# Optimization experiments

Measured on AMD Instinct MI355X. Metric: run time of the kernel, lower is better.

Reference implementation:

```python
import jax, jax.numpy as jnp
import numpy as np

P = 2048       # output dim (genes)
D = 64         # latent dim
H1, H2 = 512, 512  # n_neurons
E = 16         # num_experts
N = 2048       # batch
GATE_H = 64    # gate hidden width


def _glorot(key, shape):
    fan_in, fan_out = shape[-2], shape[-1]
    lim = jnp.sqrt(6.0 / (fan_in + fan_out)).astype(jnp.float32)
    return jax.random.uniform(key, shape, jnp.float32, -lim, lim)


def setup_inputs() -> dict:
    key = jax.random.key(0)
    ks = jax.random.split(key, 12)
    z = jax.random.normal(ks[0], (N, D), jnp.float32)
    # stacked per-expert MLP weights: d -> H1 -> H2 -> p
    W1 = _glorot(ks[1], (E, D, H1));  b1 = jnp.zeros((E, H1), jnp.float32)
    W2 = _glorot(ks[2], (E, H1, H2)); b2 = jnp.zeros((E, H2), jnp.float32)
    W3 = _glorot(ks[3], (E, H2, P));  b3 = jnp.zeros((E, P), jnp.float32)
    # gate network: d -> 64 -> E
    Wg1 = _glorot(ks[4], (D, GATE_H)); bg1 = jnp.zeros((GATE_H,), jnp.float32)
    Wg2 = _glorot(ks[5], (GATE_H, E)); bg2 = jnp.zeros((E,), jnp.float32)
    # expert assignment matrix A: [p, E], binary; ensure no all-zero row
    u = jax.random.uniform(ks[6], (P, E))
    A = jnp.where(u < 0.5, 1.0, 0.0).astype(jnp.float32)
    A = A.at[:, 0].set(1.0)
    return {"z": z, "W1": W1, "b1": b1, "W2": W2, "b2": b2,
            "W3": W3, "b3": b3, "Wg1": Wg1, "bg1": bg1,
            "Wg2": Wg2, "bg2": bg2, "A": A}


def reference(z, W1, b1, W2, b2, W3, b3, Wg1, bg1, Wg2, bg2, A):
    # experts, batched across E (replaces Python loop over nn.ModuleList)
    h = jax.nn.relu(jnp.einsum('nd,edh->neh', z, W1) + b1[None])      # [N,E,H1]
    h = jax.nn.relu(jnp.einsum('neh,ehk->nek', h, W2) + b2[None])     # [N,E,H2]
    expert_out = jnp.einsum('nek,ekp->nep', h, W3) + b3[None]         # [N,E,P]
    # gate network + softmax over experts
    g = jax.nn.relu(z @ Wg1 + bg1) @ Wg2 + bg2                        # [N,E]
    gate = jax.nn.softmax(g, axis=1)                                  # [N,E]
    # feature-wise gating: gate[n,e] * A[p,e], normalized over experts
    fw = gate[:, None, :] * A[None, :, :]                             # [N,P,E]
    fw = fw / (jnp.sum(fw, axis=2, keepdims=True) + 1e-8)
    # weighted combine: sum_e expert_out[n,e,p] * fw[n,p,e]
    x_rec = jnp.einsum('nep,npe->np', expert_out, fw)                 # [N,P]
    return (x_rec, fw)
```

## Files before the change

kernel.cpp:

```cpp
#include <hip/hip_runtime.h>
#include <hip/hip_bf16.h>

#define NN   2048
#define DD   64
#define HH1  512
#define HH2  512
#define PP   2048
#define EE   16
#define KBIG (EE * HH2)

typedef unsigned short ushort_t;
typedef __attribute__((ext_vector_type(8))) short bf16x8;
typedef __attribute__((ext_vector_type(4))) float f32x4;

__device__ __forceinline__ float b2f(ushort_t u) {
  union { unsigned int i; float f; } v; v.i = ((unsigned int)u) << 16; return v.f;
}
__device__ __forceinline__ ushort_t f2b(float f) {
  union { float f; unsigned int i; } v; v.f = f;
  unsigned int x = v.i;
  unsigned int r = (x + 0x7fffu + ((x >> 16) & 1u)) >> 16;
  return (ushort_t)r;
}
__device__ __forceinline__ float ldf(const void* p, size_t i, int isb) {
  return isb ? b2f(((const ushort_t*)p)[i]) : ((const float*)p)[i];
}

__device__ __forceinline__ void async16(ushort_t* lds, const ushort_t* g) {
  __builtin_amdgcn_global_load_lds(
      (const __attribute__((address_space(1))) void*)g,
      (__attribute__((address_space(3))) void*)lds, 16, 0, 0);
}

__device__ __forceinline__ int xcd_swz(int orig, int nwg) {
  int q = nwg >> 3, r = nwg & 7;
  int xcd = orig & 7, loc = orig >> 3;
  return (xcd < r ? xcd * (q + 1) : r * (q + 1) + (xcd - r) * q) + loc;
}

__global__ void k_sniff(const unsigned int* __restrict__ zraw,
                        int* __restrict__ flag) {
  __shared__ int cnt[256];
  int t = threadIdx.x;
  int c = 0;
  for (int i = t; i < 1024; i += 256) {
    unsigned int u = zraw[i];
    unsigned int e = (u >> 7) & 0xFFu;
    c += (e >= 110u && e <= 135u) ? 1 : 0;
  }
  cnt[t] = c;
  __syncthreads();
  for (int s = 128; s > 0; s >>= 1) {
    if (t < s) cnt[t] += cnt[t + s];
    __syncthreads();
  }
  if (t == 0) *flag = (cnt[0] >= 512) ? 1 : 0;
}

__global__ void k_probe(int* __restrict__ mapflag) {
  __shared__ ushort_t Ap[16 * 32];
  __shared__ ushort_t Bp[16 * 32];
  int t = threadIdx.x;
  for (int i = t; i < 512; i += 64) {
    int r = i >> 5, k = i & 31;
    Ap[i] = f2b((float)((r + k) % 7));
    Bp[i] = f2b((float)((2 * r + k) % 5));
  }
  __syncthreads();
  int lr = t & 15, quad = t >> 4;
  bf16x8 a = *(const bf16x8*)&Ap[lr * 32 + quad * 8];
  bf16x8 b = *(const bf16x8*)&Bp[lr * 32 + quad * 8];
  f32x4 acc = {};
  acc = __builtin_amdgcn_mfma_f32_16x16x32_bf16(a, b, acc, 0, 0, 0);
  bool m0 = true, m1 = true;
  for (int r = 0; r < 4; ++r) {
    float r0 = 0.f, r1 = 0.f;
    for (int k = 0; k < 32; ++k) {
      r0 += (float)(((quad * 4 + r) + k) % 7) * (float)((2 * lr + k) % 5);
      r1 += (float)((lr + k) % 7) * (float)((2 * (quad * 4 + r) + k) % 5);
    }
    m0 &= fabsf(acc[r] - r0) < 0.5f;
    m1 &= fabsf(acc[r] - r1) < 0.5f;
  }
  unsigned long long b0 = __ballot(m0);
  unsigned long long b1 = __ballot(m1);
  if (t == 0) *mapflag = (b0 == ~0ULL) ? 0 : ((b1 == ~0ULL) ? 1 : 0);
}

__global__ void k_convert(const void* __restrict__ src,
                          ushort_t* __restrict__ dst, int n,
                          const int* __restrict__ flag) {
  int isb = *flag;
  int stride = gridDim.x * blockDim.x;
  for (int g = blockIdx.x * blockDim.x + threadIdx.x; g * 8 < n; g += stride) {
    int base = g * 8;
    ushort_t ov[8];
    if (isb) {
      *(uint4*)ov = *(const uint4*)((const ushort_t*)src + base);
    } else {
      const float* s = (const float*)src + base;
      float4 f0 = *(const float4*)s;
      float4 f1 = *(const float4*)(s + 4);
      ov[0] = f2b(f0.x); ov[1] = f2b(f0.y); ov[2] = f2b(f0.z); ov[3] = f2b(f0.w);
      ov[4] = f2b(f1.x); ov[5] = f2b(f1.y); ov[6] = f2b(f1.z); ov[7] = f2b(f1.w);
    }
    *(uint4*)(dst + base) = *(uint4*)ov;
  }
}

__global__ void k_transpose_cvt(const void* __restrict__ src_,
                                ushort_t* __restrict__ dst, int K, int H,
                                int ld_dst, long e_dst_off,
                                const void* __restrict__ Amask,
                                const int* __restrict__ flag) {
  __shared__ ushort_t tile[64][68];
  int isb = *flag;
  int e = blockIdx.z;
  size_t ebase = (size_t)e * K * H;
  dst += (size_t)e * e_dst_off;
  int h0 = blockIdx.x * 64, k0 = blockIdx.y * 64;
  int t = threadIdx.x;
#pragma unroll
  for (int it = 0; it < 2; ++it) {
    int c = it * 256 + t;
    int row = c >> 3, col = (c & 7) * 8;
    size_t idx = ebase + (size_t)(k0 + row) * H + h0 + col;
    ushort_t tmp[8];
    if (isb) {
      *(uint4*)tmp = *(const uint4*)((const ushort_t*)src_ + idx);
    } else {
      const float* s = (const float*)src_ + idx;
      float4 f0 = *(const float4*)s;
      float4 f1 = *(const float4*)(s + 4);
      tmp[0] = f2b(f0.x); tmp[1] = f2b(f0.y); tmp[2] = f2b(f0.z); tmp[3] = f2b(f0.w);
      tmp[4] = f2b(f1.x); tmp[5] = f2b(f1.y); tmp[6] = f2b(f1.z); tmp[7] = f2b(f1.w);
    }
#pragma unroll
    for (int j = 0; j < 8; ++j) tile[row][col + j] = tmp[j];
  }
  __syncthreads();
#pragma unroll
  for (int it = 0; it < 2; ++it) {
    int c = it * 256 + t;
    int row = c >> 3, col = (c & 7) * 8;
    ushort_t tmp[8];
#pragma unroll
    for (int j = 0; j < 8; ++j) tmp[j] = tile[col + j][row];
    if (Amask) {
      float a = ldf(Amask, (size_t)(h0 + row) * EE + e, isb);
#pragma unroll
      for (int j = 0; j < 8; ++j) tmp[j] = f2b(a * b2f(tmp[j]));
    }
    *(uint4*)(dst + (size_t)(h0 + row) * ld_dst + k0 + col) = *(uint4*)tmp;
  }
}

__global__ void k_gate(const void* __restrict__ z,
                       const void* __restrict__ Wg1,
                       const void* __restrict__ bg1,
                       const void* __restrict__ Wg2,
                       const void* __restrict__ bg2,
                       const int* __restrict__ flag,
                       float* __restrict__ gate) {
  __shared__ float sW1[64][65];
  __shared__ float sW2[64][16];
  __shared__ float sb1[64];
  __shared__ float sb2[16];
  __shared__ float sz[4][64];
  __shared__ float shid[4][64];
  __shared__ float sg[4][16];
  int isb = *flag;
  int t = threadIdx.x;
  for (int i = t; i < 64 * 64; i += 256) sW1[i >> 6][i & 63] = ldf(Wg1, i, isb);
  for (int i = t; i < 64 * 16; i += 256) sW2[i >> 4][i & 15] = ldf(Wg2, i, isb);
  if (t < 64) sb1[t] = ldf(bg1, t, isb);
  if (t < 16) sb2[t] = ldf(bg2, t, isb);
  int w = t >> 6, l = t & 63;
  int n = blockIdx.x * 4 + w;
  sz[w][l] = ldf(z, (size_t)n * DD + l, isb);
  __syncthreads();
  float acc = sb1[l];
#pragma unroll
  for (int d = 0; d < 64; ++d) acc += sz[w][d] * sW1[d][l];
  shid[w][l] = fmaxf(acc, 0.f);
  __syncthreads();
  if (l < 16) {
    float g = sb2[l];
#pragma unroll
    for (int j = 0; j < 64; ++j) g += shid[w][j] * sW2[j][l];
    sg[w][l] = g;
  }
  __syncthreads();
  if (l < 16) {
    float m = -1e30f;
    for (int e2 = 0; e2 < 16; ++e2) m = fmaxf(m, sg[w][e2]);
    float s = 0.f;
    for (int e2 = 0; e2 < 16; ++e2) s += __expf(sg[w][e2] - m);
    gate[(size_t)n * EE + l] = __expf(sg[w][l] - m) / s;
  }
}

__global__ __launch_bounds__(256) void k_gemm_bt_relu(
    const ushort_t* __restrict__ Aact, const ushort_t* __restrict__ Bt,
    const ushort_t* __restrict__ bias, ushort_t* __restrict__ Cout,
    int M, int K, int ldc,
    long a_stride_e, long b_stride_e, long bias_stride_e, long c_stride_e,
    const float* __restrict__ gs,
    const int* __restrict__ mapflag) {
  __shared__ ushort_t As[2][128 * 32];
  __shared__ ushort_t Bs[2][128 * 32];
  int e = blockIdx.z;
  Aact += (size_t)e * a_stride_e;
  Bt   += (size_t)e * b_stride_e;
  bias += (size_t)e * bias_stride_e;
  Cout += (size_t)e * c_stride_e;
  int nxy = gridDim.x * gridDim.y;
  int swz = xcd_swz(blockIdx.x + gridDim.x * blockIdx.y, nxy);
  int m0 = (swz / gridDim.x) * 128, n0 = (swz % gridDim.x) * 128;
  int t = threadIdx.x;
  int w = t >> 6, l = t & 63;
  int wm = (w >> 1) * 64, wn = (w & 1) * 64;
  int lr = l & 15, quad = l >> 4;
  int mf = *mapflag;

  f32x4 acc[4][4] = {};
#pragma unroll
  for (int it = 0; it < 2; ++it) {
    int c = it * 256 + t;
    int row = c >> 2, kk = (c & 3) * 8;
    async16(&As[0][row * 32 + kk], Aact + (size_t)(m0 + row) * K + kk);
    async16(&Bs[0][row * 32 + kk], Bt + (size_t)(n0 + row) * K + kk);
  }
  __syncthreads();
  int cur = 0;
  for (int k0 = 0; k0 < K; k0 += 32) {
    if (k0 + 32 < K) {
      int nxt = cur ^ 1;
#pragma unroll
      for (int it = 0; it < 2; ++it) {
        int c = it * 256 + t;
        int row = c >> 2, kk = (c & 3) * 8;
        async16(&As[nxt][row * 32 + kk],
                Aact + (size_t)(m0 + row) * K + k0 + 32 + kk);
        async16(&Bs[nxt][row * 32 + kk],
                Bt + (size_t)(n0 + row) * K + k0 + 32 + kk);
      }
    }
    bf16x8 af[4], bfr[4];
#pragma unroll
    for (int i = 0; i < 4; ++i)
      af[i] = *(const bf16x8*)&As[cur][(wm + i * 16 + lr) * 32 + quad * 8];
#pragma unroll
    for (int j = 0; j < 4; ++j)
      bfr[j] = *(const bf16x8*)&Bs[cur][(wn + j * 16 + lr) * 32 + quad * 8];
#pragma unroll
    for (int i = 0; i < 4; ++i)
#pragma unroll
      for (int j = 0; j < 4; ++j)
        acc[i][j] = __builtin_amdgcn_mfma_f32_16x16x32_bf16(af[i], bfr[j],
                                                            acc[i][j], 0, 0, 0);
    __syncthreads();
    cur ^= 1;
  }
  if (mf == 0) {
    float gv[4][4];
#pragma unroll
    for (int i = 0; i < 4; ++i)
#pragma unroll
      for (int r = 0; r < 4; ++r)
        gv[i][r] = gs ? gs[(size_t)(m0 + wm + i * 16 + quad * 4 + r) * EE + e]
                      : 1.f;
#pragma unroll
    for (int j = 0; j < 4; ++j) {
      int n = n0 + wn + j * 16 + lr;
      float bv = b2f(bias[n]);
#pragma unroll
      for (int i = 0; i < 4; ++i)
#pragma unroll
        for (int r = 0; r < 4; ++r) {
          int m = m0 + wm + i * 16 + quad * 4 + r;
          Cout[(size_t)m * ldc + n] =
              f2b(fmaxf(acc[i][j][r] + bv, 0.f) * gv[i][r]);
        }
    }
  } else {
#pragma unroll
    for (int i = 0; i < 4; ++i) {
      int m = m0 + wm + i * 16 + lr;
      float gvi = gs ? gs[(size_t)m * EE + e] : 1.f;
#pragma unroll
      for (int j = 0; j < 4; ++j)
#pragma unroll
        for (int r = 0; r < 4; ++r) {
          int n = n0 + wn + j * 16 + quad * 4 + r;
          Cout[(size_t)m * ldc + n] =
              f2b(fmaxf(acc[i][j][r] + b2f(bias[n]), 0.f) * gvi);
        }
    }
  }
}

__global__ __launch_bounds__(256) void k_bigk(
    const ushort_t* __restrict__ Ab,
    const ushort_t* __restrict__ Bb,
    float* __restrict__ part,
    int splits,
    const int* __restrict__ mapflag) {
  __shared__ ushort_t As[2][128 * 32];
  __shared__ ushort_t Bs[2][128 * 32];
  int s = blockIdx.z;
  int nxy = gridDim.x * gridDim.y;
  int swz = xcd_swz(blockIdx.x + gridDim.x * blockIdx.y, nxy);
  int m0 = (swz / gridDim.x) * 128, n0 = (swz % gridDim.x) * 128;
  int t = threadIdx.x;
  int w = t >> 6, l = t & 63;
  int wm = (w >> 1) * 64, wn = (w & 1) * 64;
  int lr = l & 15, quad = l >> 4;
  int mf = *mapflag;
  float* out = part + (size_t)s * NN * PP;
  int kspan = KBIG / splits;
  int kbeg = s * kspan, kend = kbeg + kspan;

  f32x4 acc[4][4] = {};
#pragma unroll
  for (int it = 0; it < 2; ++it) {
    int c = it * 256 + t;
    int row = c >> 2, kk = (c & 3) * 8;
    async16(&As[0][row * 32 + kk], Ab + (size_t)(m0 + row) * KBIG + kbeg + kk);
    async16(&Bs[0][row * 32 + kk], Bb + (size_t)(n0 + row) * KBIG + kbeg + kk);
  }
  __syncthreads();
  int cur = 0;
  for (int k0 = kbeg; k0 < kend; k0 += 32) {
    if (k0 + 32 < kend) {
      int nxt = cur ^ 1;
#pragma unroll
      for (int it = 0; it < 2; ++it) {
        int c = it * 256 + t;
        int row = c >> 2, kk = (c & 3) * 8;
        async16(&As[nxt][row * 32 + kk],
                Ab + (size_t)(m0 + row) * KBIG + k0 + 32 + kk);
        async16(&Bs[nxt][row * 32 + kk],
                Bb + (size_t)(n0 + row) * KBIG + k0 + 32 + kk);
      }
    }
    bf16x8 af[4], bfr[4];
#pragma unroll
    for (int i = 0; i < 4; ++i)
      af[i] = *(const bf16x8*)&As[cur][(wm + i * 16 + lr) * 32 + quad * 8];
#pragma unroll
    for (int j = 0; j < 4; ++j)
      bfr[j] = *(const bf16x8*)&Bs[cur][(wn + j * 16 + lr) * 32 + quad * 8];
#pragma unroll
    for (int i = 0; i < 4; ++i)
#pragma unroll
      for (int j = 0; j < 4; ++j)
        acc[i][j] = __builtin_amdgcn_mfma_f32_16x16x32_bf16(af[i], bfr[j],
                                                            acc[i][j], 0, 0, 0);
    __syncthreads();
    cur ^= 1;
  }
  if (mf == 0) {
#pragma unroll
    for (int j = 0; j < 4; ++j) {
      int n = n0 + wn + j * 16 + lr;
#pragma unroll
      for (int i = 0; i < 4; ++i)
#pragma unroll
        for (int r = 0; r < 4; ++r) {
          int m = m0 + wm + i * 16 + quad * 4 + r;
          out[(size_t)m * PP + n] = acc[i][j][r];
        }
    }
  } else {
#pragma unroll
    for (int i = 0; i < 4; ++i) {
      int m = m0 + wm + i * 16 + lr;
#pragma unroll
      for (int j = 0; j < 4; ++j)
#pragma unroll
        for (int r = 0; r < 4; ++r) {
          int n = n0 + wn + j * 16 + quad * 4 + r;
          out[(size_t)m * PP + n] = acc[i][j][r];
        }
    }
  }
}

__global__ __launch_bounds__(256) void k_fw_final(
    const float* __restrict__ gate,
    const ushort_t* __restrict__ Amat,
    const ushort_t* __restrict__ b3,
    const float* __restrict__ part,
    int splits,
    float* __restrict__ xrec,
    float* __restrict__ fw) {
  size_t stride = (size_t)gridDim.x * blockDim.x;
  for (size_t i = (size_t)blockIdx.x * blockDim.x + threadIdx.x;
       i < (size_t)NN * PP; i += stride) {
    int n = (int)(i >> 11);
    int p = (int)(i & (PP - 1));
    uint4 a0 = *(const uint4*)(Amat + (size_t)p * EE);
    uint4 a1 = *(const uint4*)(Amat + (size_t)p * EE + 8);
    ushort_t av[16];
    *(uint4*)av = a0;
    *(uint4*)(av + 8) = a1;
    float wv[16];
    float s = 0.f, bias = 0.f;
#pragma unroll
    for (int e = 0; e < 16; ++e) {
      wv[e] = gate[(size_t)n * EE + e] * b2f(av[e]);
      s += wv[e];
      bias += wv[e] * b2f(b3[(size_t)e * PP + p]);
    }
    float num = bias;
    for (int sp = 0; sp < splits; ++sp) num += part[(size_t)sp * NN * PP + i];
    float inv = 1.f / (s + 1e-8f);
    xrec[i] = num * inv;
    float* dst = fw + i * EE;
#pragma unroll
    for (int e = 0; e < 16; ++e) wv[e] *= inv;
    *(float4*)(dst + 0)  = *(float4*)(wv + 0);
    *(float4*)(dst + 4)  = *(float4*)(wv + 4);
    *(float4*)(dst + 8)  = *(float4*)(wv + 8);
    *(float4*)(dst + 12) = *(float4*)(wv + 12);
  }
}

extern "C" void kernel_launch(void* const* d_in, const int* in_sizes, int n_in,
                              void* d_out, int out_size, void* d_ws,
                              size_t ws_size, hipStream_t stream) {
  const void* z_r   = d_in[0];
  const void* W1_r  = d_in[1];
  const void* b1_r  = d_in[2];
  const void* W2_r  = d_in[3];
  const void* b2_r  = d_in[4];
  const void* W3_r  = d_in[5];
  const void* b3_r  = d_in[6];
  const void* Wg1_r = d_in[7];
  const void* bg1_r = d_in[8];
  const void* Wg2_r = d_in[9];
  const void* bg2_r = d_in[10];
  const void* A_r   = d_in[11];

  float* xrec = (float*)d_out;
  float* fw   = (float*)d_out + (size_t)NN * PP;

  char* ws = (char*)d_ws;
  int* flag    = (int*)ws;             ws += 128;
  int* mapflag = (int*)ws;             ws += 128;
  float* gate = (float*)ws;            ws += (size_t)NN * EE * 4;
  ushort_t* zC   = (ushort_t*)ws;      ws += (size_t)NN * DD * 2;
  ushort_t* b1C  = (ushort_t*)ws;      ws += (size_t)EE * HH1 * 2;
  ushort_t* b2C  = (ushort_t*)ws;      ws += (size_t)EE * HH2 * 2;
  ushort_t* b3C  = (ushort_t*)ws;      ws += (size_t)EE * PP * 2;
  ushort_t* AC   = (ushort_t*)ws;      ws += (size_t)PP * EE * 2;
  ushort_t* W1t = (ushort_t*)ws;       ws += (size_t)EE * HH1 * DD * 2;
  ushort_t* W2t = (ushort_t*)ws;       ws += (size_t)EE * HH2 * HH1 * 2;
  ushort_t* W3big = (ushort_t*)ws;     ws += (size_t)PP * KBIG * 2;
  ushort_t* H2big = (ushort_t*)ws;     ws += (size_t)NN * KBIG * 2;
  ushort_t* h1  = (ushort_t*)ws;       ws += (size_t)EE * NN * HH1 * 2;
  float* partial = (float*)h1;
  size_t off_h1 = (size_t)((char*)h1 - (char*)d_ws);
  int splits = (ws_size >= off_h1 + (size_t)4 * NN * PP * 4) ? 4 : 2;

  k_sniff<<<1, 256, 0, stream>>>((const unsigned int*)z_r, flag);
  k_probe<<<1, 64, 0, stream>>>(mapflag);

  auto cvt = [&](const void* src, ushort_t* dst, int n) {
    int blocks = (n / 8 + 255) / 256;
    if (blocks < 1) blocks = 1;
    k_convert<<<blocks, 256, 0, stream>>>(src, dst, n, flag);
  };
  cvt(z_r,  zC,  NN * DD);
  cvt(b1_r, b1C, EE * HH1);
  cvt(b2_r, b2C, EE * HH2);
  cvt(b3_r, b3C, EE * PP);
  cvt(A_r,  AC,  PP * EE);

  k_transpose_cvt<<<dim3(HH1 / 64, DD / 64, EE), 256, 0, stream>>>(
      W1_r, W1t, DD, HH1, DD, (long)HH1 * DD, nullptr, flag);
  k_transpose_cvt<<<dim3(HH2 / 64, HH1 / 64, EE), 256, 0, stream>>>(
      W2_r, W2t, HH1, HH2, HH1, (long)HH2 * HH1, nullptr, flag);
  k_transpose_cvt<<<dim3(PP / 64, HH2 / 64, EE), 256, 0, stream>>>(
      W3_r, W3big, HH2, PP, KBIG, (long)HH2, A_r, flag);

  k_gate<<<NN / 4, 256, 0, stream>>>(z_r, Wg1_r, bg1_r, Wg2_r, bg2_r, flag, gate);

  k_gemm_bt_relu<<<dim3(HH1 / 128, NN / 128, EE), 256, 0, stream>>>(
      zC, W1t, b1C, h1, NN, DD, HH1,
      0, (long)HH1 * DD, HH1, (long)NN * HH1, nullptr, mapflag);
  k_gemm_bt_relu<<<dim3(HH2 / 128, NN / 128, EE), 256, 0, stream>>>(
      h1, W2t, b2C, H2big, NN, HH1, KBIG,
      (long)NN * HH1, (long)HH2 * HH1, HH2, (long)HH2, gate, mapflag);

  k_bigk<<<dim3(PP / 128, NN / 128, splits), 256, 0, stream>>>(
      H2big, W3big, partial, splits, mapflag);

  k_fw_final<<<2048, 256, 0, stream>>>(
      gate, AC, b3C, partial, splits, xrec, fw);
}
```

Measured before the change: 610.2 us.

## Use 256x256 tiles for big GEMMs, merge setup kernels, drop double buffering

```diff
diff --git a/kernel.cpp b/kernel.cpp
--- a/kernel.cpp
+++ b/kernel.cpp
@@ -32,15 +32,11 @@
       (__attribute__((address_space(3))) void*)lds, 16, 0, 0);
 }
 
-__device__ __forceinline__ int xcd_swz(int orig, int nwg) {
-  int q = nwg >> 3, r = nwg & 7;
-  int xcd = orig & 7, loc = orig >> 3;
-  return (xcd < r ? xcd * (q + 1) : r * (q + 1) + (xcd - r) * q) + loc;
-}
-
-__global__ void k_sniff(const unsigned int* __restrict__ zraw,
-                        int* __restrict__ flag) {
+__global__ void k_init(const unsigned int* __restrict__ zraw,
+                       int* __restrict__ flag, int* __restrict__ mapflag) {
   __shared__ int cnt[256];
+  __shared__ ushort_t Ap[16 * 32];
+  __shared__ ushort_t Bp[16 * 32];
   int t = threadIdx.x;
   int c = 0;
   for (int i = t; i < 1024; i += 256) {
@@ -55,50 +51,65 @@
     __syncthreads();
   }
   if (t == 0) *flag = (cnt[0] >= 512) ? 1 : 0;
-}
-
-__global__ void k_probe(int* __restrict__ mapflag) {
-  __shared__ ushort_t Ap[16 * 32];
-  __shared__ ushort_t Bp[16 * 32];
-  int t = threadIdx.x;
-  for (int i = t; i < 512; i += 64) {
-    int r = i >> 5, k = i & 31;
-    Ap[i] = f2b((float)((r + k) % 7));
-    Bp[i] = f2b((float)((2 * r + k) % 5));
+  if (t < 64) {
+    for (int i = t; i < 512; i += 64) {
+      int r = i >> 5, k = i & 31;
+      Ap[i] = f2b((float)((r + k) % 7));
+      Bp[i] = f2b((float)((2 * r + k) % 5));
+    }
   }
   __syncthreads();
-  int lr = t & 15, quad = t >> 4;
-  bf16x8 a = *(const bf16x8*)&Ap[lr * 32 + quad * 8];
-  bf16x8 b = *(const bf16x8*)&Bp[lr * 32 + quad * 8];
-  f32x4 acc = {};
-  acc = __builtin_amdgcn_mfma_f32_16x16x32_bf16(a, b, acc, 0, 0, 0);
-  bool m0 = true, m1 = true;
-  for (int r = 0; r < 4; ++r) {
-    float r0 = 0.f, r1 = 0.f;
-    for (int k = 0; k < 32; ++k) {
-      r0 += (float)(((quad * 4 + r) + k) % 7) * (float)((2 * lr + k) % 5);
-      r1 += (float)((lr + k) % 7) * (float)((2 * (quad * 4 + r) + k) % 5);
-    }
-    m0 &= fabsf(acc[r] - r0) < 0.5f;
-    m1 &= fabsf(acc[r] - r1) < 0.5f;
-  }
-  unsigned long long b0 = __ballot(m0);
-  unsigned long long b1 = __ballot(m1);
-  if (t == 0) *mapflag = (b0 == ~0ULL) ? 0 : ((b1 == ~0ULL) ? 1 : 0);
-}
-
-__global__ void k_convert(const void* __restrict__ src,
-                          ushort_t* __restrict__ dst, int n,
-                          const int* __restrict__ flag) {
+  if (t < 64) {
+    int lr = t & 15, quad = t >> 4;
+    bf16x8 a = *(const bf16x8*)&Ap[lr * 32 + quad * 8];
+    bf16x8 b = *(const bf16x8*)&Bp[lr * 32 + quad * 8];
+    f32x4 acc = {};
+    acc = __builtin_amdgcn_mfma_f32_16x16x32_bf16(a, b, acc, 0, 0, 0);
+    bool m0 = true, m1 = true;
+    for (int r = 0; r < 4; ++r) {
+      float r0 = 0.f, r1 = 0.f;
+      for (int k = 0; k < 32; ++k) {
+        r0 += (float)(((quad * 4 + r) + k) % 7) * (float)((2 * lr + k) % 5);
+        r1 += (float)((lr + k) % 7) * (float)((2 * (quad * 4 + r) + k) % 5);
+      }
+      m0 &= fabsf(acc[r] - r0) < 0.5f;
+      m1 &= fabsf(acc[r] - r1) < 0.5f;
+    }
+    unsigned long long b0 = __ballot(m0);
+    unsigned long long b1 = __ballot(m1);
+    if (t == 0) *mapflag = (b0 == ~0ULL) ? 0 : ((b1 == ~0ULL) ? 1 : 0);
+  }
+}
+
+#define CVT_O1 (NN * DD)
+#define CVT_O2 (CVT_O1 + EE * HH1)
+#define CVT_O3 (CVT_O2 + EE * HH2)
+#define CVT_O4 (CVT_O3 + EE * PP)
+#define CVT_O5 (CVT_O4 + PP * EE)
+__global__ void k_convert5(const void* __restrict__ s0,
+                           const void* __restrict__ s1,
+                           const void* __restrict__ s2,
+                           const void* __restrict__ s3,
+                           const void* __restrict__ s4,
+                           ushort_t* __restrict__ dst,
+                           const int* __restrict__ flag) {
   int isb = *flag;
   int stride = gridDim.x * blockDim.x;
-  for (int g = blockIdx.x * blockDim.x + threadIdx.x; g * 8 < n; g += stride) {
+  for (int g = blockIdx.x * blockDim.x + threadIdx.x; g * 8 < CVT_O5;
+       g += stride) {
     int base = g * 8;
+    const void* src;
+    int off;
+    if (base < CVT_O1)      { src = s0; off = base; }
+    else if (base < CVT_O2) { src = s1; off = base - CVT_O1; }
+    else if (base < CVT_O3) { src = s2; off = base - CVT_O2; }
+    else if (base < CVT_O4) { src = s3; off = base - CVT_O3; }
+    else                    { src = s4; off = base - CVT_O4; }
     ushort_t ov[8];
     if (isb) {
-      *(uint4*)ov = *(const uint4*)((const ushort_t*)src + base);
+      *(uint4*)ov = *(const uint4*)((const ushort_t*)src + off);
     } else {
-      const float* s = (const float*)src + base;
+      const float* s = (const float*)src + off;
       float4 f0 = *(const float4*)s;
       float4 f1 = *(const float4*)(s + 4);
       ov[0] = f2b(f0.x); ov[1] = f2b(f0.y); ov[2] = f2b(f0.z); ov[3] = f2b(f0.w);
@@ -207,16 +218,14 @@
     long a_stride_e, long b_stride_e, long bias_stride_e, long c_stride_e,
     const float* __restrict__ gs,
     const int* __restrict__ mapflag) {
-  __shared__ ushort_t As[2][128 * 32];
-  __shared__ ushort_t Bs[2][128 * 32];
+  __shared__ ushort_t As[128 * 32];
+  __shared__ ushort_t Bs[128 * 32];
   int e = blockIdx.z;
   Aact += (size_t)e * a_stride_e;
   Bt   += (size_t)e * b_stride_e;
   bias += (size_t)e * bias_stride_e;
   Cout += (size_t)e * c_stride_e;
-  int nxy = gridDim.x * gridDim.y;
-  int swz = xcd_swz(blockIdx.x + gridDim.x * blockIdx.y, nxy);
-  int m0 = (swz / gridDim.x) * 128, n0 = (swz % gridDim.x) * 128;
+  int m0 = blockIdx.y * 128, n0 = blockIdx.x * 128;
   int t = threadIdx.x;
   int w = t >> 6, l = t & 63;
   int wm = (w >> 1) * 64, wn = (w & 1) * 64;
@@ -224,35 +233,27 @@
   int mf = *mapflag;
 
   f32x4 acc[4][4] = {};
-#pragma unroll
-  for (int it = 0; it < 2; ++it) {
-    int c = it * 256 + t;
-    int row = c >> 2, kk = (c & 3) * 8;
-    async16(&As[0][row * 32 + kk], Aact + (size_t)(m0 + row) * K + kk);
-    async16(&Bs[0][row * 32 + kk], Bt + (size_t)(n0 + row) * K + kk);
-  }
-  __syncthreads();
-  int cur = 0;
   for (int k0 = 0; k0 < K; k0 += 32) {
-    if (k0 + 32 < K) {
-      int nxt = cur ^ 1;
-#pragma unroll
-      for (int it = 0; it < 2; ++it) {
-        int c = it * 256 + t;
-        int row = c >> 2, kk = (c & 3) * 8;
-        async16(&As[nxt][row * 32 + kk],
-                Aact + (size_t)(m0 + row) * K + k0 + 32 + kk);
-        async16(&Bs[nxt][row * 32 + kk],
-                Bt + (size_t)(n0 + row) * K + k0 + 32 + kk);
-      }
-    }
+#pragma unroll
+    for (int it = 0; it < 2; ++it) {
+      int c = it * 256 + t;
+      int row = c >> 2, kk = (c & 3) * 8;
+      async16(&As[row * 32 + kk], Aact + (size_t)(m0 + row) * K + k0 + kk);
+    }
+#pragma unroll
+    for (int it = 0; it < 2; ++it) {
+      int c = it * 256 + t;
+      int row = c >> 2, kk = (c & 3) * 8;
+      async16(&Bs[row * 32 + kk], Bt + (size_t)(n0 + row) * K + k0 + kk);
+    }
+    __syncthreads();
     bf16x8 af[4], bfr[4];
 #pragma unroll
     for (int i = 0; i < 4; ++i)
-      af[i] = *(const bf16x8*)&As[cur][(wm + i * 16 + lr) * 32 + quad * 8];
+      af[i] = *(const bf16x8*)&As[(wm + i * 16 + lr) * 32 + quad * 8];
 #pragma unroll
     for (int j = 0; j < 4; ++j)
-      bfr[j] = *(const bf16x8*)&Bs[cur][(wn + j * 16 + lr) * 32 + quad * 8];
+      bfr[j] = *(const bf16x8*)&Bs[(wn + j * 16 + lr) * 32 + quad * 8];
 #pragma unroll
     for (int i = 0; i < 4; ++i)
 #pragma unroll
@@ -260,7 +261,6 @@
         acc[i][j] = __builtin_amdgcn_mfma_f32_16x16x32_bf16(af[i], bfr[j],
                                                             acc[i][j], 0, 0, 0);
     __syncthreads();
-    cur ^= 1;
   }
   if (mf == 0) {
     float gv[4][4];
@@ -300,81 +300,160 @@
   }
 }
 
-__global__ __launch_bounds__(256) void k_bigk(
+
+#define STAGE256(dstLDS, srcBase, ldK)                                       \
+  {                                                                          \
+    _Pragma("unroll") for (int it = 0; it < 4; ++it) {                       \
+      int c = it * 512 + t;                                                  \
+      int row = c >> 3, kk = (c & 7) * 8;                                    \
+      async16(&dstLDS[row * 64 + kk], srcBase + (size_t)row * ldK + kk);     \
+    }                                                                        \
+  }
+
+__global__ __launch_bounds__(512) void k_gemm256_relu(
+    const ushort_t* __restrict__ Aact, const ushort_t* __restrict__ Bt,
+    const ushort_t* __restrict__ bias, ushort_t* __restrict__ Cout,
+    int K, int ldc,
+    long a_stride_e, long b_stride_e, long bias_stride_e, long c_stride_e,
+    const float* __restrict__ gs,
+    const int* __restrict__ mapflag) {
+  __shared__ ushort_t As[256 * 64];
+  __shared__ ushort_t Bs[256 * 64];
+  int e = blockIdx.z;
+  Aact += (size_t)e * a_stride_e;
+  Bt   += (size_t)e * b_stride_e;
+  bias += (size_t)e * bias_stride_e;
+  Cout += (size_t)e * c_stride_e;
+  int m0 = blockIdx.y * 256, n0 = blockIdx.x * 256;
+  int t = threadIdx.x;
+  int w = t >> 6, l = t & 63;
+  int wm = (w >> 2) * 128, wn = (w & 3) * 64;
+  int lr = l & 15, quad = l >> 4;
+  int mf = *mapflag;
+
+  f32x4 acc[8][4] = {};
+  for (int k0 = 0; k0 < K; k0 += 64) {
+    const ushort_t* aSrc = Aact + (size_t)m0 * K + k0;
+    const ushort_t* bSrc = Bt + (size_t)n0 * K + k0;
+    STAGE256(As, aSrc, K);
+    STAGE256(Bs, bSrc, K);
+    __syncthreads();
+#pragma unroll
+    for (int h = 0; h < 2; ++h) {
+      int kc = h * 32 + quad * 8;
+      bf16x8 af[8], bfr[4];
+#pragma unroll
+      for (int i = 0; i < 8; ++i)
+        af[i] = *(const bf16x8*)&As[(wm + i * 16 + lr) * 64 + kc];
+#pragma unroll
+      for (int j = 0; j < 4; ++j)
+        bfr[j] = *(const bf16x8*)&Bs[(wn + j * 16 + lr) * 64 + kc];
+#pragma unroll
+      for (int i = 0; i < 8; ++i)
+#pragma unroll
+        for (int j = 0; j < 4; ++j)
+          acc[i][j] = __builtin_amdgcn_mfma_f32_16x16x32_bf16(
+              af[i], bfr[j], acc[i][j], 0, 0, 0);
+    }
+    __syncthreads();
+  }
+  if (mf == 0) {
+#pragma unroll
+    for (int i = 0; i < 8; ++i) {
+      float gv[4];
+#pragma unroll
+      for (int r = 0; r < 4; ++r)
+        gv[r] = gs ? gs[(size_t)(m0 + wm + i * 16 + quad * 4 + r) * EE + e]
+                   : 1.f;
+#pragma unroll
+      for (int j = 0; j < 4; ++j) {
+        int n = n0 + wn + j * 16 + lr;
+        float bv = b2f(bias[n]);
+#pragma unroll
+        for (int r = 0; r < 4; ++r) {
+          int m = m0 + wm + i * 16 + quad * 4 + r;
+          Cout[(size_t)m * ldc + n] =
+              f2b(fmaxf(acc[i][j][r] + bv, 0.f) * gv[r]);
+        }
+      }
+    }
+  } else {
+#pragma unroll
+    for (int i = 0; i < 8; ++i) {
+      int m = m0 + wm + i * 16 + lr;
+      float gvi = gs ? gs[(size_t)m * EE + e] : 1.f;
+#pragma unroll
+      for (int j = 0; j < 4; ++j)
+#pragma unroll
+        for (int r = 0; r < 4; ++r) {
+          int n = n0 + wn + j * 16 + quad * 4 + r;
+          Cout[(size_t)m * ldc + n] =
+              f2b(fmaxf(acc[i][j][r] + b2f(bias[n]), 0.f) * gvi);
+        }
+    }
+  }
+}
+
+__global__ __launch_bounds__(512) void k_bigk256(
     const ushort_t* __restrict__ Ab,
     const ushort_t* __restrict__ Bb,
     float* __restrict__ part,
     int splits,
     const int* __restrict__ mapflag) {
-  __shared__ ushort_t As[2][128 * 32];
-  __shared__ ushort_t Bs[2][128 * 32];
+  __shared__ ushort_t As[256 * 64];
+  __shared__ ushort_t Bs[256 * 64];
   int s = blockIdx.z;
-  int nxy = gridDim.x * gridDim.y;
-  int swz = xcd_swz(blockIdx.x + gridDim.x * blockIdx.y, nxy);
-  int m0 = (swz / gridDim.x) * 128, n0 = (swz % gridDim.x) * 128;
+  int m0 = blockIdx.y * 256, n0 = blockIdx.x * 256;
   int t = threadIdx.x;
   int w = t >> 6, l = t & 63;
-  int wm = (w >> 1) * 64, wn = (w & 1) * 64;
+  int wm = (w >> 2) * 128, wn = (w & 3) * 64;
   int lr = l & 15, quad = l >> 4;
   int mf = *mapflag;
   float* out = part + (size_t)s * NN * PP;
   int kspan = KBIG / splits;
   int kbeg = s * kspan, kend = kbeg + kspan;
 
-  f32x4 acc[4][4] = {};
-#pragma unroll
-  for (int it = 0; it < 2; ++it) {
-    int c = it * 256 + t;
-    int row = c >> 2, kk = (c & 3) * 8;
-    async16(&As[0][row * 32 + kk], Ab + (size_t)(m0 + row) * KBIG + kbeg + kk);
-    async16(&Bs[0][row * 32 + kk], Bb + (size_t)(n0 + row) * KBIG + kbeg + kk);
-  }
-  __syncthreads();
-  int cur = 0;
-  for (int k0 = kbeg; k0 < kend; k0 += 32) {
-    if (k0 + 32 < kend) {
-      int nxt = cur ^ 1;
-#pragma unroll
-      for (int it = 0; it < 2; ++it) {
-        int c = it * 256 + t;
-        int row = c >> 2, kk = (c & 3) * 8;
-        async16(&As[nxt][row * 32 + kk],
-                Ab + (size_t)(m0 + row) * KBIG + k0 + 32 + kk);
-        async16(&Bs[nxt][row * 32 + kk],
-                Bb + (size_t)(n0 + row) * KBIG + k0 + 32 + kk);
-      }
-    }
-    bf16x8 af[4], bfr[4];
-#pragma unroll
-    for (int i = 0; i < 4; ++i)
-      af[i] = *(const bf16x8*)&As[cur][(wm + i * 16 + lr) * 32 + quad * 8];
-#pragma unroll
-    for (int j = 0; j < 4; ++j)
-      bfr[j] = *(const bf16x8*)&Bs[cur][(wn + j * 16 + lr) * 32 + quad * 8];
-#pragma unroll
-    for (int i = 0; i < 4; ++i)
+  f32x4 acc[8][4] = {};
+  for (int k0 = kbeg; k0 < kend; k0 += 64) {
+    const ushort_t* aSrc = Ab + (size_t)m0 * KBIG + k0;
+    const ushort_t* bSrc = Bb + (size_t)n0 * KBIG + k0;
+    STAGE256(As, aSrc, KBIG);
+    STAGE256(Bs, bSrc, KBIG);
+    __syncthreads();
+#pragma unroll
+    for (int h = 0; h < 2; ++h) {
+      int kc = h * 32 + quad * 8;
+      bf16x8 af[8], bfr[4];
+#pragma unroll
+      for (int i = 0; i < 8; ++i)
+        af[i] = *(const bf16x8*)&As[(wm + i * 16 + lr) * 64 + kc];
 #pragma unroll
       for (int j = 0; j < 4; ++j)
-        acc[i][j] = __builtin_amdgcn_mfma_f32_16x16x32_bf16(af[i], bfr[j],
-                                                            acc[i][j], 0, 0, 0);
-    __syncthreads();
-    cur ^= 1;
+        bfr[j] = *(const bf16x8*)&Bs[(wn + j * 16 + lr) * 64 + kc];
+#pragma unroll
+      for (int i = 0; i < 8; ++i)
+#pragma unroll
+        for (int j = 0; j < 4; ++j)
+          acc[i][j] = __builtin_amdgcn_mfma_f32_16x16x32_bf16(
+              af[i], bfr[j], acc[i][j], 0, 0, 0);
+    }
+    __syncthreads();
   }
   if (mf == 0) {
 #pragma unroll
-    for (int j = 0; j < 4; ++j) {
-      int n = n0 + wn + j * 16 + lr;
-#pragma unroll
-      for (int i = 0; i < 4; ++i)
+    for (int i = 0; i < 8; ++i)
+#pragma unroll
+      for (int j = 0; j < 4; ++j) {
+        int n = n0 + wn + j * 16 + lr;
 #pragma unroll
         for (int r = 0; r < 4; ++r) {
           int m = m0 + wm + i * 16 + quad * 4 + r;
           out[(size_t)m * PP + n] = acc[i][j][r];
         }
-    }
+      }
   } else {
 #pragma unroll
-    for (int i = 0; i < 4; ++i) {
+    for (int i = 0; i < 8; ++i) {
       int m = m0 + wm + i * 16 + lr;
 #pragma unroll
       for (int j = 0; j < 4; ++j)
@@ -464,19 +543,9 @@
   size_t off_h1 = (size_t)((char*)h1 - (char*)d_ws);
   int splits = (ws_size >= off_h1 + (size_t)4 * NN * PP * 4) ? 4 : 2;
 
-  k_sniff<<<1, 256, 0, stream>>>((const unsigned int*)z_r, flag);
-  k_probe<<<1, 64, 0, stream>>>(mapflag);
-
-  auto cvt = [&](const void* src, ushort_t* dst, int n) {
-    int blocks = (n / 8 + 255) / 256;
-    if (blocks < 1) blocks = 1;
-    k_convert<<<blocks, 256, 0, stream>>>(src, dst, n, flag);
-  };
-  cvt(z_r,  zC,  NN * DD);
-  cvt(b1_r, b1C, EE * HH1);
-  cvt(b2_r, b2C, EE * HH2);
-  cvt(b3_r, b3C, EE * PP);
-  cvt(A_r,  AC,  PP * EE);
+  k_init<<<1, 256, 0, stream>>>((const unsigned int*)z_r, flag, mapflag);
+
+  k_convert5<<<104, 256, 0, stream>>>(z_r, b1_r, b2_r, b3_r, A_r, zC, flag);
 
   k_transpose_cvt<<<dim3(HH1 / 64, DD / 64, EE), 256, 0, stream>>>(
       W1_r, W1t, DD, HH1, DD, (long)HH1 * DD, nullptr, flag);
@@ -490,11 +559,11 @@
   k_gemm_bt_relu<<<dim3(HH1 / 128, NN / 128, EE), 256, 0, stream>>>(
       zC, W1t, b1C, h1, NN, DD, HH1,
       0, (long)HH1 * DD, HH1, (long)NN * HH1, nullptr, mapflag);
-  k_gemm_bt_relu<<<dim3(HH2 / 128, NN / 128, EE), 256, 0, stream>>>(
-      h1, W2t, b2C, H2big, NN, HH1, KBIG,
+  k_gemm256_relu<<<dim3(HH2 / 256, NN / 256, EE), 512, 0, stream>>>(
+      h1, W2t, b2C, H2big, HH1, KBIG,
       (long)NN * HH1, (long)HH2 * HH1, HH2, (long)HH2, gate, mapflag);
 
-  k_bigk<<<dim3(PP / 128, NN / 128, splits), 256, 0, stream>>>(
+  k_bigk256<<<dim3(PP / 256, NN / 256, splits), 512, 0, stream>>>(
       H2big, W3big, partial, splits, mapflag);
 
   k_fw_final<<<2048, 256, 0, stream>>>(
```

New measurement: 615.9 us. About the same (+0.9%).

## Merge setup kernels, drop XCD swizzle, and simplify GEMM staging addressing

Applied to the files above, without the earlier changes.

```diff
diff --git a/kernel.cpp b/kernel.cpp
--- a/kernel.cpp
+++ b/kernel.cpp
@@ -32,15 +32,11 @@
       (__attribute__((address_space(3))) void*)lds, 16, 0, 0);
 }
 
-__device__ __forceinline__ int xcd_swz(int orig, int nwg) {
-  int q = nwg >> 3, r = nwg & 7;
-  int xcd = orig & 7, loc = orig >> 3;
-  return (xcd < r ? xcd * (q + 1) : r * (q + 1) + (xcd - r) * q) + loc;
-}
-
-__global__ void k_sniff(const unsigned int* __restrict__ zraw,
-                        int* __restrict__ flag) {
+__global__ void k_init(const unsigned int* __restrict__ zraw,
+                       int* __restrict__ flag, int* __restrict__ mapflag) {
   __shared__ int cnt[256];
+  __shared__ ushort_t Ap[16 * 32];
+  __shared__ ushort_t Bp[16 * 32];
   int t = threadIdx.x;
   int c = 0;
   for (int i = t; i < 1024; i += 256) {
@@ -55,50 +51,65 @@
     __syncthreads();
   }
   if (t == 0) *flag = (cnt[0] >= 512) ? 1 : 0;
-}
-
-__global__ void k_probe(int* __restrict__ mapflag) {
-  __shared__ ushort_t Ap[16 * 32];
-  __shared__ ushort_t Bp[16 * 32];
-  int t = threadIdx.x;
-  for (int i = t; i < 512; i += 64) {
-    int r = i >> 5, k = i & 31;
-    Ap[i] = f2b((float)((r + k) % 7));
-    Bp[i] = f2b((float)((2 * r + k) % 5));
-  }
-  __syncthreads();
-  int lr = t & 15, quad = t >> 4;
-  bf16x8 a = *(const bf16x8*)&Ap[lr * 32 + quad * 8];
-  bf16x8 b = *(const bf16x8*)&Bp[lr * 32 + quad * 8];
-  f32x4 acc = {};
-  acc = __builtin_amdgcn_mfma_f32_16x16x32_bf16(a, b, acc, 0, 0, 0);
-  bool m0 = true, m1 = true;
-  for (int r = 0; r < 4; ++r) {
-    float r0 = 0.f, r1 = 0.f;
-    for (int k = 0; k < 32; ++k) {
-      r0 += (float)(((quad * 4 + r) + k) % 7) * (float)((2 * lr + k) % 5);
-      r1 += (float)((lr + k) % 7) * (float)((2 * (quad * 4 + r) + k) % 5);
-    }
-    m0 &= fabsf(acc[r] - r0) < 0.5f;
-    m1 &= fabsf(acc[r] - r1) < 0.5f;
-  }
-  unsigned long long b0 = __ballot(m0);
-  unsigned long long b1 = __ballot(m1);
-  if (t == 0) *mapflag = (b0 == ~0ULL) ? 0 : ((b1 == ~0ULL) ? 1 : 0);
-}
-
-__global__ void k_convert(const void* __restrict__ src,
-                          ushort_t* __restrict__ dst, int n,
-                          const int* __restrict__ flag) {
+  if (t < 64) {
+    for (int i = t; i < 512; i += 64) {
+      int r = i >> 5, k = i & 31;
+      Ap[i] = f2b((float)((r + k) % 7));
+      Bp[i] = f2b((float)((2 * r + k) % 5));
+    }
+  }
+  __syncthreads();
+  if (t < 64) {
+    int lr = t & 15, quad = t >> 4;
+    bf16x8 a = *(const bf16x8*)&Ap[lr * 32 + quad * 8];
+    bf16x8 b = *(const bf16x8*)&Bp[lr * 32 + quad * 8];
+    f32x4 acc = {};
+    acc = __builtin_amdgcn_mfma_f32_16x16x32_bf16(a, b, acc, 0, 0, 0);
+    bool m0 = true, m1 = true;
+    for (int r = 0; r < 4; ++r) {
+      float r0 = 0.f, r1 = 0.f;
+      for (int k = 0; k < 32; ++k) {
+        r0 += (float)(((quad * 4 + r) + k) % 7) * (float)((2 * lr + k) % 5);
+        r1 += (float)((lr + k) % 7) * (float)((2 * (quad * 4 + r) + k) % 5);
+      }
+      m0 &= fabsf(acc[r] - r0) < 0.5f;
+      m1 &= fabsf(acc[r] - r1) < 0.5f;
+    }
+    unsigned long long b0 = __ballot(m0);
+    unsigned long long b1 = __ballot(m1);
+    if (t == 0) *mapflag = (b0 == ~0ULL) ? 0 : ((b1 == ~0ULL) ? 1 : 0);
+  }
+}
+
+#define CVT_O1 (NN * DD)
+#define CVT_O2 (CVT_O1 + EE * HH1)
+#define CVT_O3 (CVT_O2 + EE * HH2)
+#define CVT_O4 (CVT_O3 + EE * PP)
+#define CVT_O5 (CVT_O4 + PP * EE)
+__global__ void k_convert5(const void* __restrict__ s0,
+                           const void* __restrict__ s1,
+                           const void* __restrict__ s2,
+                           const void* __restrict__ s3,
+                           const void* __restrict__ s4,
+                           ushort_t* __restrict__ dst,
+                           const int* __restrict__ flag) {
   int isb = *flag;
   int stride = gridDim.x * blockDim.x;
-  for (int g = blockIdx.x * blockDim.x + threadIdx.x; g * 8 < n; g += stride) {
+  for (int g = blockIdx.x * blockDim.x + threadIdx.x; g * 8 < CVT_O5;
+       g += stride) {
     int base = g * 8;
+    const void* src;
+    int off;
+    if (base < CVT_O1)      { src = s0; off = base; }
+    else if (base < CVT_O2) { src = s1; off = base - CVT_O1; }
+    else if (base < CVT_O3) { src = s2; off = base - CVT_O2; }
+    else if (base < CVT_O4) { src = s3; off = base - CVT_O3; }
+    else                    { src = s4; off = base - CVT_O4; }
     ushort_t ov[8];
     if (isb) {
-      *(uint4*)ov = *(const uint4*)((const ushort_t*)src + base);
+      *(uint4*)ov = *(const uint4*)((const ushort_t*)src + off);
     } else {
-      const float* s = (const float*)src + base;
+      const float* s = (const float*)src + off;
       float4 f0 = *(const float4*)s;
       float4 f1 = *(const float4*)(s + 4);
       ov[0] = f2b(f0.x); ov[1] = f2b(f0.y); ov[2] = f2b(f0.z); ov[3] = f2b(f0.w);
@@ -200,10 +211,20 @@
   }
 }
 
+#define STAGE128(dstA, dstB, aSrc, bSrc, ldA, ldB)                           \
+  {                                                                          \
+    _Pragma("unroll") for (int it = 0; it < 2; ++it) {                       \
+      int c = it * 256 + t;                                                  \
+      int row = c >> 2, kk = (c & 3) * 8;                                    \
+      async16(&dstA[row * 32 + kk], aSrc + (size_t)row * ldA + kk);          \
+      async16(&dstB[row * 32 + kk], bSrc + (size_t)row * ldB + kk);          \
+    }                                                                        \
+  }
+
 __global__ __launch_bounds__(256) void k_gemm_bt_relu(
     const ushort_t* __restrict__ Aact, const ushort_t* __restrict__ Bt,
     const ushort_t* __restrict__ bias, ushort_t* __restrict__ Cout,
-    int M, int K, int ldc,
+    int K, int ldc,
     long a_stride_e, long b_stride_e, long bias_stride_e, long c_stride_e,
     const float* __restrict__ gs,
     const int* __restrict__ mapflag) {
@@ -214,9 +235,7 @@
   Bt   += (size_t)e * b_stride_e;
   bias += (size_t)e * bias_stride_e;
   Cout += (size_t)e * c_stride_e;
-  int nxy = gridDim.x * gridDim.y;
-  int swz = xcd_swz(blockIdx.x + gridDim.x * blockIdx.y, nxy);
-  int m0 = (swz / gridDim.x) * 128, n0 = (swz % gridDim.x) * 128;
+  int m0 = blockIdx.y * 128, n0 = blockIdx.x * 128;
   int t = threadIdx.x;
   int w = t >> 6, l = t & 63;
   int wm = (w >> 1) * 64, wn = (w & 1) * 64;
@@ -224,27 +243,17 @@
   int mf = *mapflag;
 
   f32x4 acc[4][4] = {};
-#pragma unroll
-  for (int it = 0; it < 2; ++it) {
-    int c = it * 256 + t;
-    int row = c >> 2, kk = (c & 3) * 8;
-    async16(&As[0][row * 32 + kk], Aact + (size_t)(m0 + row) * K + kk);
-    async16(&Bs[0][row * 32 + kk], Bt + (size_t)(n0 + row) * K + kk);
-  }
+  const ushort_t* aBase = Aact + (size_t)m0 * K;
+  const ushort_t* bBase = Bt + (size_t)n0 * K;
+  STAGE128(As[0], Bs[0], aBase, bBase, K, K);
   __syncthreads();
   int cur = 0;
-  for (int k0 = 0; k0 < K; k0 += 32) {
-    if (k0 + 32 < K) {
-      int nxt = cur ^ 1;
-#pragma unroll
-      for (int it = 0; it < 2; ++it) {
-        int c = it * 256 + t;
-        int row = c >> 2, kk = (c & 3) * 8;
-        async16(&As[nxt][row * 32 + kk],
-                Aact + (size_t)(m0 + row) * K + k0 + 32 + kk);
-        async16(&Bs[nxt][row * 32 + kk],
-                Bt + (size_t)(n0 + row) * K + k0 + 32 + kk);
-      }
+  int nt = K >> 5;
+  for (int ti = 0; ti < nt; ++ti) {
+    if (ti + 1 < nt) {
+      const ushort_t* aN = aBase + (ti + 1) * 32;
+      const ushort_t* bN = bBase + (ti + 1) * 32;
+      STAGE128(As[cur ^ 1], Bs[cur ^ 1], aN, bN, K, K);
     }
     bf16x8 af[4], bfr[4];
 #pragma unroll
@@ -309,9 +318,7 @@
   __shared__ ushort_t As[2][128 * 32];
   __shared__ ushort_t Bs[2][128 * 32];
   int s = blockIdx.z;
-  int nxy = gridDim.x * gridDim.y;
-  int swz = xcd_swz(blockIdx.x + gridDim.x * blockIdx.y, nxy);
-  int m0 = (swz / gridDim.x) * 128, n0 = (swz % gridDim.x) * 128;
+  int m0 = blockIdx.y * 128, n0 = blockIdx.x * 128;
   int t = threadIdx.x;
   int w = t >> 6, l = t & 63;
   int wm = (w >> 1) * 64, wn = (w & 1) * 64;
@@ -319,30 +326,20 @@
   int mf = *mapflag;
   float* out = part + (size_t)s * NN * PP;
   int kspan = KBIG / splits;
-  int kbeg = s * kspan, kend = kbeg + kspan;
+  int kbeg = s * kspan;
 
   f32x4 acc[4][4] = {};
-#pragma unroll
-  for (int it = 0; it < 2; ++it) {
-    int c = it * 256 + t;
-    int row = c >> 2, kk = (c & 3) * 8;
-    async16(&As[0][row * 32 + kk], Ab + (size_t)(m0 + row) * KBIG + kbeg + kk);
-    async16(&Bs[0][row * 32 + kk], Bb + (size_t)(n0 + row) * KBIG + kbeg + kk);
-  }
+  const ushort_t* aBase = Ab + (size_t)m0 * KBIG + kbeg;
+  const ushort_t* bBase = Bb + (size_t)n0 * KBIG + kbeg;
+  STAGE128(As[0], Bs[0], aBase, bBase, KBIG, KBIG);
   __syncthreads();
   int cur = 0;
-  for (int k0 = kbeg; k0 < kend; k0 += 32) {
-    if (k0 + 32 < kend) {
-      int nxt = cur ^ 1;
-#pragma unroll
-      for (int it = 0; it < 2; ++it) {
-        int c = it * 256 + t;
-        int row = c >> 2, kk = (c & 3) * 8;
-        async16(&As[nxt][row * 32 + kk],
-                Ab + (size_t)(m0 + row) * KBIG + k0 + 32 + kk);
-        async16(&Bs[nxt][row * 32 + kk],
-                Bb + (size_t)(n0 + row) * KBIG + k0 + 32 + kk);
-      }
+  int nt = kspan >> 5;
+  for (int ti = 0; ti < nt; ++ti) {
+    if (ti + 1 < nt) {
+      const ushort_t* aN = aBase + (ti + 1) * 32;
+      const ushort_t* bN = bBase + (ti + 1) * 32;
+      STAGE128(As[cur ^ 1], Bs[cur ^ 1], aN, bN, KBIG, KBIG);
     }
     bf16x8 af[4], bfr[4];
 #pragma unroll
@@ -464,19 +461,9 @@
   size_t off_h1 = (size_t)((char*)h1 - (char*)d_ws);
   int splits = (ws_size >= off_h1 + (size_t)4 * NN * PP * 4) ? 4 : 2;
 
-  k_sniff<<<1, 256, 0, stream>>>((const unsigned int*)z_r, flag);
-  k_probe<<<1, 64, 0, stream>>>(mapflag);
-
-  auto cvt = [&](const void* src, ushort_t* dst, int n) {
-    int blocks = (n / 8 + 255) / 256;
-    if (blocks < 1) blocks = 1;
-    k_convert<<<blocks, 256, 0, stream>>>(src, dst, n, flag);
-  };
-  cvt(z_r,  zC,  NN * DD);
-  cvt(b1_r, b1C, EE * HH1);
-  cvt(b2_r, b2C, EE * HH2);
-  cvt(b3_r, b3C, EE * PP);
-  cvt(A_r,  AC,  PP * EE);
+  k_init<<<1, 256, 0, stream>>>((const unsigned int*)z_r, flag, mapflag);
+
+  k_convert5<<<104, 256, 0, stream>>>(z_r, b1_r, b2_r, b3_r, A_r, zC, flag);
 
   k_transpose_cvt<<<dim3(HH1 / 64, DD / 64, EE), 256, 0, stream>>>(
       W1_r, W1t, DD, HH1, DD, (long)HH1 * DD, nullptr, flag);
@@ -488,10 +475,10 @@
   k_gate<<<NN / 4, 256, 0, stream>>>(z_r, Wg1_r, bg1_r, Wg2_r, bg2_r, flag, gate);
 
   k_gemm_bt_relu<<<dim3(HH1 / 128, NN / 128, EE), 256, 0, stream>>>(
-      zC, W1t, b1C, h1, NN, DD, HH1,
+      zC, W1t, b1C, h1, DD, HH1,
       0, (long)HH1 * DD, HH1, (long)NN * HH1, nullptr, mapflag);
   k_gemm_bt_relu<<<dim3(HH2 / 128, NN / 128, EE), 256, 0, stream>>>(
-      h1, W2t, b2C, H2big, NN, HH1, KBIG,
+      h1, W2t, b2C, H2big, HH1, KBIG,
       (long)NN * HH1, (long)HH2 * HH1, HH2, (long)HH2, gate, mapflag);
 
   k_bigk<<<dim3(PP / 128, NN / 128, splits), 256, 0, stream>>>(
```

Result: no change. 610.6 us (+0.1%).
